# Kernel tuning notes

Measured on AMD Instinct MI355X. Metric: run time of the kernel, lower is better.

Reference implementation:

```python
import jax, jax.numpy as jnp
import numpy as np

W_WIDTH = 2048   # neurons per topological batch
N_BATCH = 9      # number of non-input topological batches
NUM_IN = W_WIDTH # input neurons


def setup_inputs() -> dict:
    key = jax.random.key(0)
    k_x, k_w, k_b = jax.random.split(key, 3)
    scale = 1.0 / jnp.sqrt(jnp.float32(W_WIDTH))
    x = jax.random.normal(k_x, (W_WIDTH,), dtype=jnp.float32)
    weights = jax.random.normal(k_w, (N_BATCH, W_WIDTH, W_WIDTH), dtype=jnp.float32) * scale
    bias = jax.random.normal(k_b, (N_BATCH * W_WIDTH,), dtype=jnp.float32) * 0.01
    masks = jnp.ones((N_BATCH, W_WIDTH, W_WIDTH), dtype=bool)
    # idx for topo batch i = ids of previous layer = [i*W, (i+1)*W)
    idxs = jnp.arange(N_BATCH * W_WIDTH, dtype=jnp.int64 if jax.config.jax_enable_x64 else jnp.int32).reshape(N_BATCH, W_WIDTH)
    return {"x": x, "weights": weights, "bias": bias, "masks": masks, "idxs": idxs}


def reference(x, weights, bias, masks, idxs):
    W = x.shape[0]
    L = weights.shape[0]
    num_neurons = (L + 1) * W
    # dropout_p = 0 -> dropout_keep is all ones; input neurons get x directly
    values = jnp.zeros((num_neurons,), dtype=x.dtype).at[:W].set(x)
    for i in range(L):  # fixed small loop over topological batches
        gathered = values[idxs[i]]                                   # gather [W]
        eff_w = weights[i] * masks[i].astype(x.dtype)                # masked weights [W, W]
        affine = eff_w @ gathered + bias[i * W:(i + 1) * W]          # affine [W]
        # hidden batches use silu; the final batch is the output neurons (identity elem act)
        out = jax.nn.silu(affine) if i < L - 1 else affine
        values = values.at[(i + 1) * W:(i + 2) * W].set(out)         # scatter
    # output_activation_group = identity
    return values[L * W:]
```

## Files before the change

kernel.cpp:

```cpp
#include <hip/hip_runtime.h>


#define W_WIDTH  2048
#define TPB      512
#define N_WAVES  (TPB / 64)
#define NBLOCKS  (W_WIDTH / N_WAVES)
#define N_LAYERS 9

typedef float v4f __attribute__((ext_vector_type(4)));

__device__ __forceinline__ void issue_weights(const float* wrow_lane,
                                              v4f* wn, float* br,
                                              const float* bptr)
{
    const float* b0 = wrow_lane;
    const float* b1 = wrow_lane + 1024;
    asm volatile("global_load_dwordx4 %0, %1, off nt"             : "=v"(wn[0]) : "v"(b0) : "memory");
    asm volatile("global_load_dwordx4 %0, %1, off offset:1024 nt" : "=v"(wn[1]) : "v"(b0) : "memory");
    asm volatile("global_load_dwordx4 %0, %1, off offset:2048 nt" : "=v"(wn[2]) : "v"(b0) : "memory");
    asm volatile("global_load_dwordx4 %0, %1, off offset:3072 nt" : "=v"(wn[3]) : "v"(b0) : "memory");
    asm volatile("global_load_dwordx4 %0, %1, off nt"             : "=v"(wn[4]) : "v"(b1) : "memory");
    asm volatile("global_load_dwordx4 %0, %1, off offset:1024 nt" : "=v"(wn[5]) : "v"(b1) : "memory");
    asm volatile("global_load_dwordx4 %0, %1, off offset:2048 nt" : "=v"(wn[6]) : "v"(b1) : "memory");
    asm volatile("global_load_dwordx4 %0, %1, off offset:3072 nt" : "=v"(wn[7]) : "v"(b1) : "memory");
    asm volatile("global_load_dword %0, %1, off"                  : "=v"(*br)   : "v"(bptr) : "memory");
}

__global__ __launch_bounds__(TPB)
void mlp_fused(const float* __restrict__ x,
               const float* __restrict__ wgt,
               const float* __restrict__ bias,
               float*       __restrict__ vals,
               float*       __restrict__ out,
               unsigned*    __restrict__ cnt,
               unsigned*    __restrict__ go)
{
    __shared__ __align__(16) float xs[W_WIDTH];
    const int tid  = threadIdx.x;
    const int lane = tid & 63;
    const int wv   = tid >> 6;
    const int row  = blockIdx.x * N_WAVES + wv;
    const int goln = (blockIdx.x & 7) * 32;

    v4f   wbuf[2][8];
    float br[2];
    v4f   av;

    issue_weights(wgt + (size_t)row * W_WIDTH + lane * 4, wbuf[0], &br[0],
                  bias + row);
    {
        const float* ap = x + 4 * tid;
        asm volatile("global_load_dwordx4 %0, %1, off" : "=v"(av) : "v"(ap) : "memory");
    }

    #pragma unroll
    for (int i = 0; i < N_LAYERS; ++i) {
        asm volatile("s_waitcnt vmcnt(0)" ::: "memory");
        __builtin_amdgcn_sched_barrier(0);

        *(v4f*)&xs[4 * tid] = av;
        __syncthreads();

        float acc = 0.f;
        const v4f* xv = (const v4f*)xs;
        #pragma unroll
        for (int k = 0; k < 8; ++k) {
            v4f wk = wbuf[i & 1][k];
            v4f xk = xv[k * 64 + lane];
            acc = fmaf(wk.x, xk.x, acc);
            acc = fmaf(wk.y, xk.y, acc);
            acc = fmaf(wk.z, xk.z, acc);
            acc = fmaf(wk.w, xk.w, acc);
        }
        #pragma unroll
        for (int off = 32; off > 0; off >>= 1)
            acc += __shfl_xor(acc, off, 64);
        float a = acc + br[i & 1];

        if (i == N_LAYERS - 1) {
            if (lane == 0) out[row] = a;
        } else {
            if (lane == 0) {
                float s = a / (1.f + __expf(-a));
                const float* vp = vals + (size_t)i * W_WIDTH + row;
                asm volatile("global_store_dword %0, %1, off sc0 sc1"
                             :: "v"(vp), "v"(s) : "memory");
            }

            issue_weights(wgt + ((size_t)(i + 1) * W_WIDTH + row) * W_WIDTH + lane * 4,
                          wbuf[(i + 1) & 1], &br[(i + 1) & 1],
                          bias + (size_t)(i + 1) * W_WIDTH + row);

            asm volatile("s_waitcnt vmcnt(9)" ::: "memory");
            __builtin_amdgcn_sched_barrier(0);
            __builtin_amdgcn_s_barrier();

            if (tid == 0) {
                unsigned old = __hip_atomic_fetch_add(
                    cnt, 1u, __ATOMIC_RELAXED, __HIP_MEMORY_SCOPE_AGENT);
                if (old == (unsigned)(NBLOCKS * (i + 1) - 1)) {
                    #pragma unroll
                    for (int j = 0; j < 8; ++j)
                        __hip_atomic_store(&go[j * 32], (unsigned)(i + 1),
                                           __ATOMIC_RELAXED,
                                           __HIP_MEMORY_SCOPE_AGENT);
                }
                while (__hip_atomic_load(&go[goln], __ATOMIC_RELAXED,
                                         __HIP_MEMORY_SCOPE_AGENT)
                       < (unsigned)(i + 1))
                    __builtin_amdgcn_s_sleep(2);
            }
            __builtin_amdgcn_s_barrier();

            const float* ap = vals + (size_t)i * W_WIDTH + 4 * tid;
            asm volatile("global_load_dwordx4 %0, %1, off sc0 sc1"
                         : "=v"(av) : "v"(ap) : "memory");
        }
    }
}

extern "C" void kernel_launch(void* const* d_in, const int* in_sizes, int n_in,
                              void* d_out, int out_size, void* d_ws, size_t ws_size,
                              hipStream_t stream)
{
    (void)in_sizes; (void)n_in; (void)out_size; (void)ws_size;

    const float* x    = (const float*)d_in[0];
    const float* wgt  = (const float*)d_in[1];
    const float* bias = (const float*)d_in[2];
    float*       out  = (float*)d_out;

    float*    vals = (float*)d_ws;
    char*     barb = (char*)d_ws + (size_t)(N_LAYERS - 1) * W_WIDTH * sizeof(float);
    unsigned* cnt  = (unsigned*)barb;
    unsigned* go   = (unsigned*)(barb + 128);

    hipMemsetAsync(barb, 0, 1152, stream);

    mlp_fused<<<dim3(NBLOCKS), dim3(TPB), 0, stream>>>(
        x, wgt, bias, vals, out, cnt, go);
}
```

Measured before the change: 295.1 us.

## Replace atomic grid barrier with stamped data packets polled per layer

Each block now writes its activations together with a layer stamp into a double-buffered record array, and every thread polls the packets it needs until all stamps match. This replaces the atomic counter plus broadcast flag barrier and the separate reload of activations. The next layer's weight prefetch is also issued at the start of each layer instead of after the compute. In exchange every thread repeatedly polls global memory with coherent loads, which adds load traffic during the wait, and the stamp check depends on the packet store being visible as a single 16-byte unit.

After: 279.3 us. 5.4% less time.

```diff
diff --git a/kernel.cpp b/kernel.cpp
--- a/kernel.cpp
+++ b/kernel.cpp
@@ -7,7 +7,8 @@
 #define NBLOCKS  (W_WIDTH / N_WAVES)
 #define N_LAYERS 9
 
-typedef float v4f __attribute__((ext_vector_type(4)));
+typedef float    v4f __attribute__((ext_vector_type(4)));
+typedef unsigned v4u __attribute__((ext_vector_type(4)));
 
 __device__ __forceinline__ void issue_weights(const float* wrow_lane,
                                               v4f* wn, float* br,
@@ -30,36 +31,37 @@
 void mlp_fused(const float* __restrict__ x,
                const float* __restrict__ wgt,
                const float* __restrict__ bias,
-               float*       __restrict__ vals,
                float*       __restrict__ out,
-               unsigned*    __restrict__ cnt,
-               unsigned*    __restrict__ go)
+               unsigned*    __restrict__ rec)
 {
     __shared__ __align__(16) float xs[W_WIDTH];
+    __shared__ float arow[N_WAVES];
     const int tid  = threadIdx.x;
     const int lane = tid & 63;
     const int wv   = tid >> 6;
     const int row  = blockIdx.x * N_WAVES + wv;
-    const int goln = (blockIdx.x & 7) * 32;
 
     v4f   wbuf[2][8];
     float br[2];
-    v4f   av;
 
     issue_weights(wgt + (size_t)row * W_WIDTH + lane * 4, wbuf[0], &br[0],
                   bias + row);
+    v4f x4;
     {
         const float* ap = x + 4 * tid;
-        asm volatile("global_load_dwordx4 %0, %1, off" : "=v"(av) : "v"(ap) : "memory");
+        asm volatile("global_load_dwordx4 %0, %1, off" : "=v"(x4) : "v"(ap) : "memory");
     }
+    asm volatile("s_waitcnt vmcnt(0)" ::: "memory");
+    __builtin_amdgcn_sched_barrier(0);
+    *(v4f*)&xs[4 * tid] = x4;
+    __syncthreads();
 
     #pragma unroll
     for (int i = 0; i < N_LAYERS; ++i) {
-        asm volatile("s_waitcnt vmcnt(0)" ::: "memory");
-        __builtin_amdgcn_sched_barrier(0);
-
-        *(v4f*)&xs[4 * tid] = av;
-        __syncthreads();
+        if (i < N_LAYERS - 1)
+            issue_weights(wgt + ((size_t)(i + 1) * W_WIDTH + row) * W_WIDTH + lane * 4,
+                          wbuf[(i + 1) & 1], &br[(i + 1) & 1],
+                          bias + (size_t)(i + 1) * W_WIDTH + row);
 
         float acc = 0.f;
         const v4f* xv = (const v4f*)xs;
@@ -80,41 +82,47 @@
         if (i == N_LAYERS - 1) {
             if (lane == 0) out[row] = a;
         } else {
-            if (lane == 0) {
-                float s = a / (1.f + __expf(-a));
-                const float* vp = vals + (size_t)i * W_WIDTH + row;
-                asm volatile("global_store_dword %0, %1, off sc0 sc1"
-                             :: "v"(vp), "v"(s) : "memory");
+            if (lane == 0) arow[wv] = a / (1.f + __expf(-a));
+            asm volatile("s_waitcnt lgkmcnt(0)" ::: "memory");
+            __builtin_amdgcn_s_barrier();
+
+            const unsigned stamp = (unsigned)(i + 1);
+            unsigned* rbase = rec + ((i & 1) ? 4096 : 0);
+
+            if (wv == 0 && lane < 4) {
+                v4u pkt;
+                pkt.x = __float_as_uint(arow[2 * lane]);
+                pkt.y = __float_as_uint(arow[2 * lane + 1]);
+                pkt.z = stamp;
+                pkt.w = 0u;
+                unsigned* sp = rbase + ((size_t)blockIdx.x * 4 + lane) * 4;
+                asm volatile("global_store_dwordx4 %0, %1, off sc0 sc1"
+                             :: "v"(sp), "v"(pkt) : "memory");
             }
 
-            issue_weights(wgt + ((size_t)(i + 1) * W_WIDTH + row) * W_WIDTH + lane * 4,
-                          wbuf[(i + 1) & 1], &br[(i + 1) & 1],
-                          bias + (size_t)(i + 1) * W_WIDTH + row);
+            const unsigned* p0 = rbase + (size_t)(2 * tid) * 4;
+            const unsigned* p1 = rbase + (size_t)(2 * tid + 1) * 4;
+            v4u f0, f1;
+            for (;;) {
+                asm volatile("global_load_dwordx4 %0, %1, off sc0 sc1"
+                             : "=v"(f0) : "v"(p0) : "memory");
+                asm volatile("global_load_dwordx4 %0, %1, off sc0 sc1"
+                             : "=v"(f1) : "v"(p1) : "memory");
+                asm volatile("s_waitcnt vmcnt(0)" ::: "memory");
+                __builtin_amdgcn_sched_barrier(0);
+                bool ok = (f0.z == stamp) && (f1.z == stamp);
+                if (__all(ok)) break;
+                __builtin_amdgcn_s_sleep(1);
+            }
 
-            asm volatile("s_waitcnt vmcnt(9)" ::: "memory");
-            __builtin_amdgcn_sched_barrier(0);
+            v4f nx;
+            nx.x = __uint_as_float(f0.x);
+            nx.y = __uint_as_float(f0.y);
+            nx.z = __uint_as_float(f1.x);
+            nx.w = __uint_as_float(f1.y);
+            *(v4f*)&xs[4 * tid] = nx;
+            asm volatile("s_waitcnt lgkmcnt(0)" ::: "memory");
             __builtin_amdgcn_s_barrier();
-
-            if (tid == 0) {
-                unsigned old = __hip_atomic_fetch_add(
-                    cnt, 1u, __ATOMIC_RELAXED, __HIP_MEMORY_SCOPE_AGENT);
-                if (old == (unsigned)(NBLOCKS * (i + 1) - 1)) {
-                    #pragma unroll
-                    for (int j = 0; j < 8; ++j)
-                        __hip_atomic_store(&go[j * 32], (unsigned)(i + 1),
-                                           __ATOMIC_RELAXED,
-                                           __HIP_MEMORY_SCOPE_AGENT);
-                }
-                while (__hip_atomic_load(&go[goln], __ATOMIC_RELAXED,
-                                         __HIP_MEMORY_SCOPE_AGENT)
-                       < (unsigned)(i + 1))
-                    __builtin_amdgcn_s_sleep(2);
-            }
-            __builtin_amdgcn_s_barrier();
-
-            const float* ap = vals + (size_t)i * W_WIDTH + 4 * tid;
-            asm volatile("global_load_dwordx4 %0, %1, off sc0 sc1"
-                         : "=v"(av) : "v"(ap) : "memory");
         }
     }
 }
@@ -130,13 +138,10 @@
     const float* bias = (const float*)d_in[2];
     float*       out  = (float*)d_out;
 
-    float*    vals = (float*)d_ws;
-    char*     barb = (char*)d_ws + (size_t)(N_LAYERS - 1) * W_WIDTH * sizeof(float);
-    unsigned* cnt  = (unsigned*)barb;
-    unsigned* go   = (unsigned*)(barb + 128);
+    unsigned* rec = (unsigned*)d_ws;
 
-    hipMemsetAsync(barb, 0, 1152, stream);
+    hipMemsetAsync(rec, 0, 32768, stream);
 
     mlp_fused<<<dim3(NBLOCKS), dim3(TPB), 0, stream>>>(
-        x, wgt, bias, vals, out, cnt, go);
+        x, wgt, bias, out, rec);
 }
```
